# Optimization experiments

Measured on AMD Instinct MI355X. Metric: run time of the kernel, lower is better.

## Reference

```python
import jax, jax.numpy as jnp
import numpy as np

ALPHA = 0.01  # LeakyReLU negative slope
D_OUT = 128   # output_size; a1 is split at this index


def setup_inputs() -> dict:
    key = jax.random.key(0)
    k1, k2, k3, k4 = jax.random.split(key, 4)
    B, N, M, D_IN = 8, 2048, 2048, 256
    input_tensor1 = jax.random.normal(k1, (B, N, D_IN), dtype=jnp.float32)
    input_tensor2 = jax.random.normal(k2, (B, M, D_IN), dtype=jnp.float32)
    attention_mask2 = jnp.zeros((B, 1, M), dtype=jnp.float32)
    # Parameters (xavier-uniform-like scaled normals are fine for a numeric reference)
    W1 = jax.random.normal(k3, (D_IN, D_OUT), dtype=jnp.float32) * (1.414 * np.sqrt(2.0 / (D_IN + D_OUT)))
    a1 = jax.random.normal(k4, (2 * D_OUT, 1), dtype=jnp.float32) * (1.414 * np.sqrt(2.0 / (2 * D_OUT + 1)))
    return {"input_tensor1": input_tensor1, "input_tensor2": input_tensor2,
            "attention_mask2": attention_mask2, "W1": W1, "a1": a1}


def reference(input_tensor1, input_tensor2, attention_mask2, W1, a1):
    # Projections (dropout is identity in eval / p=0)
    Wh1 = jnp.einsum('bnd,de->bne', input_tensor1, W1)  # (B, N, E)
    Wh2 = jnp.einsum('bmd,de->bme', input_tensor2, W1)  # (B, M, E)
    # GAT-style additive score: broadcast outer-sum of two rank-1 projections
    att1 = jnp.einsum('bne,eo->bno', Wh1, a1[:D_OUT, :])   # (B, N, 1)
    att2 = jnp.einsum('bme,eo->bmo', Wh2, a1[D_OUT:, :])   # (B, M, 1)
    e = att1 + jnp.swapaxes(att2, 1, 2)                     # (B, N, M)
    e = jnp.where(e > 0, e, ALPHA * e)                      # LeakyReLU
    scores = e + attention_mask2                            # additive mask
    probs = jax.nn.softmax(scores, axis=-1)                 # (B, N, M)
    context = jnp.einsum('bnm,bme->bne', probs, Wh2)        # (B, N, E)
    return (context, probs)
```

## Files before the change

kernel.cpp:

```cpp
#include <hip/hip_runtime.h>

#define B 8
#define N 2048
#define M 2048
#define DIN 256
#define E 128
#define ALPHA 0.01f

typedef __attribute__((ext_vector_type(8))) short bf16x8;
typedef __attribute__((ext_vector_type(4))) float f32x4;

__device__ inline ushort f2bf(float x) {
  unsigned u = __float_as_uint(x);
  u = (u + 0x7FFFu + ((u >> 16) & 1u)) >> 16;
  return (ushort)u;
}

__global__ __launch_bounds__(256) void prep_v_kernel(
    const float* __restrict__ W1, const float* __restrict__ a1,
    float* __restrict__ v1, float* __restrict__ v2) {
  int k = threadIdx.x;
  float s1 = 0.f, s2 = 0.f;
#pragma unroll 8
  for (int e = 0; e < E; ++e) {
    float w = W1[k * E + e];
    s1 += w * a1[e];
    s2 += w * a1[E + e];
  }
  v1[k] = s1;
  v2[k] = s2;
}

__global__ __launch_bounds__(256) void att_kernel(
    const float* __restrict__ in1, const float* __restrict__ in2,
    const float* __restrict__ v1, const float* __restrict__ v2,
    float* __restrict__ att1, float* __restrict__ att2) {
  int wave = blockIdx.x * 4 + (threadIdx.x >> 6);
  int lane = threadIdx.x & 63;
  const float* src;
  const float* v;
  float* dst;
  int row;
  if (wave < B * N) {
    src = in1; v = v1; dst = att1; row = wave;
  } else {
    src = in2; v = v2; dst = att2; row = wave - B * N;
  }
  float4 x = *(const float4*)(src + (size_t)row * DIN + lane * 4);
  float4 vv = *(const float4*)(v + lane * 4);
  float d = x.x * vv.x + x.y * vv.y + x.z * vv.z + x.w * vv.w;
#pragma unroll
  for (int off = 32; off; off >>= 1) d += __shfl_down(d, off, 64);
  if (lane == 0) dst[row] = d;
}

__global__ __launch_bounds__(256) void wh2_kernel(
    const float* __restrict__ in2, const float* __restrict__ W1,
    ushort* __restrict__ Wb) {
  __shared__ float a[32][DIN];
  int r0 = blockIdx.x * 32;
#pragma unroll
  for (int i = 0; i < 8; ++i) {
    int f = (threadIdx.x + i * 256) * 4;
    int r = f >> 8, k = f & 255;
    *(float4*)&a[r][k] = *(const float4*)(in2 + (size_t)(r0 + r) * DIN + k);
  }
  __syncthreads();
  int c  = (threadIdx.x & 31) * 4;
  int tr = (threadIdx.x >> 5) * 4;
  float acc[4][4] = {};
  for (int k = 0; k < DIN; ++k) {
    float4 b = *(const float4*)(W1 + k * E + c);
#pragma unroll
    for (int r = 0; r < 4; ++r) {
      float av = a[tr + r][k];
      acc[r][0] += av * b.x;
      acc[r][1] += av * b.y;
      acc[r][2] += av * b.z;
      acc[r][3] += av * b.w;
    }
  }
#pragma unroll
  for (int r = 0; r < 4; ++r) {
    int m = r0 + tr + r;
    size_t gbase = (size_t)(m >> 3) * 128 * 8 + (m & 7);
#pragma unroll
    for (int j = 0; j < 4; ++j)
      Wb[gbase + (size_t)(c + j) * 8] = f2bf(acc[r][j]);
  }
}

__global__ __launch_bounds__(256) void softmax_kernel(
    const float* __restrict__ att1, const float* __restrict__ att2,
    const float* __restrict__ mask, float* __restrict__ probs) {
  int row = blockIdx.x;
  int b = row >> 11;
  float a1v = att1[row];
  __shared__ float red[8];
  float s[8];
  float mx = -1e30f;
#pragma unroll
  for (int j = 0; j < 8; ++j) {
    int m = j * 256 + threadIdx.x;
    float t = a1v + att2[b * M + m];
    t = t > 0.f ? t : ALPHA * t;
    t += mask[b * M + m];
    s[j] = t;
    mx = fmaxf(mx, t);
  }
#pragma unroll
  for (int off = 32; off; off >>= 1) mx = fmaxf(mx, __shfl_xor(mx, off, 64));
  int wid = threadIdx.x >> 6;
  if ((threadIdx.x & 63) == 0) red[wid] = mx;
  __syncthreads();
  mx = fmaxf(fmaxf(red[0], red[1]), fmaxf(red[2], red[3]));
  float sum = 0.f;
#pragma unroll
  for (int j = 0; j < 8; ++j) {
    s[j] = __expf(s[j] - mx);
    sum += s[j];
  }
#pragma unroll
  for (int off = 32; off; off >>= 1) sum += __shfl_xor(sum, off, 64);
  if ((threadIdx.x & 63) == 0) red[4 + wid] = sum;
  __syncthreads();
  sum = red[4] + red[5] + red[6] + red[7];
  float inv = 1.f / sum;
#pragma unroll
  for (int j = 0; j < 8; ++j) {
    int m = j * 256 + threadIdx.x;
    probs[(size_t)row * M + m] = s[j] * inv;
  }
}

__global__ __launch_bounds__(256) void context_kernel(
    const float* __restrict__ probs, const ushort* __restrict__ Wb,
    float* __restrict__ ctx) {
  __shared__ short ldsA[32][72];
  __shared__ ushort ldsB[8 * 128 * 8];
  int rt = blockIdx.x & 63;
  int b  = blockIdx.x >> 6;
  int row0 = b * N + rt * 32;
  int t = threadIdx.x;
  int lane = t & 63;
  int w = t >> 6;
  int quad = lane >> 4;
  int l16 = lane & 15;
  int m0w = (w & 1) * 16;
  int n0w = (w >> 1) * 64;
  int ar = t >> 3;
  int ak = (t & 7) * 8;

  f32x4 acc[4] = {};

  for (int k0 = 0; k0 < M; k0 += 64) {
    const float* ap = probs + (size_t)(row0 + ar) * M + k0 + ak;
    float4 p0 = *(const float4*)ap;
    float4 p1 = *(const float4*)(ap + 4);
    bf16x8 av;
    av[0] = (short)f2bf(p0.x); av[1] = (short)f2bf(p0.y);
    av[2] = (short)f2bf(p0.z); av[3] = (short)f2bf(p0.w);
    av[4] = (short)f2bf(p1.x); av[5] = (short)f2bf(p1.y);
    av[6] = (short)f2bf(p1.z); av[7] = (short)f2bf(p1.w);
    *(bf16x8*)&ldsA[ar][ak] = av;
    {
      const char* g =
          (const char*)(Wb + (size_t)(b * 256 + (k0 >> 3)) * 128 * 8);
      char* l = (char*)ldsB;
      int base = w * 4096 + lane * 16;
#pragma unroll
      for (int i = 0; i < 4; ++i) {
        int off = base + i * 1024;
        __builtin_amdgcn_global_load_lds(
            (const __attribute__((address_space(1))) void*)(g + off),
            (__attribute__((address_space(3))) void*)(l + off), 16, 0, 0);
      }
    }
    __syncthreads();
#pragma unroll
    for (int ks = 0; ks < 64; ks += 32) {
      bf16x8 af = *(const bf16x8*)&ldsA[m0w + l16][ks + quad * 8];
      int gl = (ks >> 3) + quad;
#pragma unroll
      for (int cf = 0; cf < 4; ++cf) {
        int n = n0w + cf * 16 + l16;
        bf16x8 bf = *(const bf16x8*)&ldsB[((size_t)gl * 128 + n) * 8];
        acc[cf] =
            __builtin_amdgcn_mfma_f32_16x16x32_bf16(af, bf, acc[cf], 0, 0, 0);
      }
    }
    __syncthreads();
  }
#pragma unroll
  for (int cf = 0; cf < 4; ++cf) {
    int nn = n0w + cf * 16 + l16;
#pragma unroll
    for (int reg = 0; reg < 4; ++reg) {
      int rr = row0 + m0w + quad * 4 + reg;
      ctx[(size_t)rr * E + nn] = acc[cf][reg];
    }
  }
}

extern "C" void kernel_launch(void* const* d_in, const int* in_sizes, int n_in,
                              void* d_out, int out_size, void* d_ws,
                              size_t ws_size, hipStream_t stream) {
  (void)in_sizes; (void)n_in; (void)out_size; (void)ws_size;
  const float* in1  = (const float*)d_in[0];
  const float* in2  = (const float*)d_in[1];
  const float* mask = (const float*)d_in[2];
  const float* W1   = (const float*)d_in[3];
  const float* a1   = (const float*)d_in[4];

  float* ws   = (float*)d_ws;
  float* v1   = ws;
  float* v2   = v1 + DIN;
  float* att1 = v2 + DIN;
  float* att2 = att1 + B * N;
  ushort* Wb  = (ushort*)(att2 + B * M);

  float* ctx   = (float*)d_out;
  float* probs = ctx + (size_t)B * N * E;

  hipLaunchKernelGGL(prep_v_kernel, dim3(1), dim3(256), 0, stream, W1, a1, v1, v2);
  hipLaunchKernelGGL(att_kernel, dim3((B * N + B * M) / 4), dim3(256), 0, stream,
                     in1, in2, v1, v2, att1, att2);
  hipLaunchKernelGGL(wh2_kernel, dim3(B * M / 32), dim3(256), 0, stream,
                     in2, W1, Wb);
  hipLaunchKernelGGL(softmax_kernel, dim3(B * N), dim3(256), 0, stream,
                     att1, att2, mask, probs);
  hipLaunchKernelGGL(context_kernel, dim3(B * N / 32), dim3(256), 0, stream,
                     probs, Wb, ctx);
}
```

Measured before the change: 248.5 us.

## Fuse softmax into context GEMM, recomputing probabilities on the fly

Merges the softmax and context kernels into one kernel. Each block stages the att2 and mask rows in LDS, computes per-row max and sum over 32 rows, then regenerates probabilities inside the MFMA loop. Those values are written to the probs output and converted to bf16 for the A operand, so the full probs matrix is no longer re-read from global memory. In exchange the exp/LeakyReLU work is done three times per element, the LDS footprint grows, and the probs stores come from only half the waves with a strided per-lane pattern.

```diff
diff --git a/kernel.cpp b/kernel.cpp
--- a/kernel.cpp
+++ b/kernel.cpp
@@ -90,79 +90,83 @@
   }
 }
 
-__global__ __launch_bounds__(256) void softmax_kernel(
+__global__ __launch_bounds__(256) void fused_kernel(
     const float* __restrict__ att1, const float* __restrict__ att2,
-    const float* __restrict__ mask, float* __restrict__ probs) {
-  int row = blockIdx.x;
-  int b = row >> 11;
-  float a1v = att1[row];
-  __shared__ float red[8];
-  float s[8];
-  float mx = -1e30f;
-#pragma unroll
-  for (int j = 0; j < 8; ++j) {
-    int m = j * 256 + threadIdx.x;
-    float t = a1v + att2[b * M + m];
-    t = t > 0.f ? t : ALPHA * t;
-    t += mask[b * M + m];
-    s[j] = t;
-    mx = fmaxf(mx, t);
-  }
-#pragma unroll
-  for (int off = 32; off; off >>= 1) mx = fmaxf(mx, __shfl_xor(mx, off, 64));
-  int wid = threadIdx.x >> 6;
-  if ((threadIdx.x & 63) == 0) red[wid] = mx;
-  __syncthreads();
-  mx = fmaxf(fmaxf(red[0], red[1]), fmaxf(red[2], red[3]));
-  float sum = 0.f;
-#pragma unroll
-  for (int j = 0; j < 8; ++j) {
-    s[j] = __expf(s[j] - mx);
-    sum += s[j];
-  }
-#pragma unroll
-  for (int off = 32; off; off >>= 1) sum += __shfl_xor(sum, off, 64);
-  if ((threadIdx.x & 63) == 0) red[4 + wid] = sum;
-  __syncthreads();
-  sum = red[4] + red[5] + red[6] + red[7];
-  float inv = 1.f / sum;
-#pragma unroll
-  for (int j = 0; j < 8; ++j) {
-    int m = j * 256 + threadIdx.x;
-    probs[(size_t)row * M + m] = s[j] * inv;
-  }
-}
-
-__global__ __launch_bounds__(256) void context_kernel(
-    const float* __restrict__ probs, const ushort* __restrict__ Wb,
-    float* __restrict__ ctx) {
-  __shared__ short ldsA[32][72];
+    const float* __restrict__ mask, const ushort* __restrict__ Wb,
+    float* __restrict__ probs, float* __restrict__ ctx) {
+  __shared__ float att2s[M];
+  __shared__ float masks[M];
+  __shared__ float att1s[32];
+  __shared__ float red[32][9];
+  __shared__ float rowmax[32];
+  __shared__ float rowinv[32];
   __shared__ ushort ldsB[8 * 128 * 8];
+
   int rt = blockIdx.x & 63;
   int b  = blockIdx.x >> 6;
   int row0 = b * N + rt * 32;
   int t = threadIdx.x;
+
+#pragma unroll
+  for (int i = 0; i < 2; ++i) {
+    int idx = (t + i * 256) * 4;
+    *(float4*)&att2s[idx] = *(const float4*)(att2 + b * M + idx);
+    *(float4*)&masks[idx] = *(const float4*)(mask + b * M + idx);
+  }
+  if (t < 32) att1s[t] = att1[row0 + t];
+  __syncthreads();
+
+  int r = t >> 3, ch = t & 7;
+  float a1r = att1s[r];
+  float mx = -1e30f;
+  for (int m = ch * 256; m < ch * 256 + 256; ++m) {
+    float s = a1r + att2s[m];
+    s = s > 0.f ? s : ALPHA * s;
+    s += masks[m];
+    mx = fmaxf(mx, s);
+  }
+  red[r][ch] = mx;
+  __syncthreads();
+  if (t < 32) {
+    float m2 = red[t][0];
+#pragma unroll
+    for (int j = 1; j < 8; ++j) m2 = fmaxf(m2, red[t][j]);
+    rowmax[t] = m2;
+  }
+  __syncthreads();
+  float rmax = rowmax[r];
+  float sum = 0.f;
+  for (int m = ch * 256; m < ch * 256 + 256; ++m) {
+    float s = a1r + att2s[m];
+    s = s > 0.f ? s : ALPHA * s;
+    s += masks[m];
+    sum += __expf(s - rmax);
+  }
+  red[r][ch] = sum;
+  __syncthreads();
+  if (t < 32) {
+    float s2 = 0.f;
+#pragma unroll
+    for (int j = 0; j < 8; ++j) s2 += red[t][j];
+    rowinv[t] = 1.f / s2;
+  }
+  __syncthreads();
+
   int lane = t & 63;
   int w = t >> 6;
   int quad = lane >> 4;
   int l16 = lane & 15;
   int m0w = (w & 1) * 16;
   int n0w = (w >> 1) * 64;
-  int ar = t >> 3;
-  int ak = (t & 7) * 8;
+  float a1v  = att1s[m0w + l16];
+  float rmxL = rowmax[m0w + l16];
+  float rinL = rowinv[m0w + l16];
+  bool do_store = (n0w == 0);
+  float* prow = probs + (size_t)(row0 + m0w + l16) * M;
 
   f32x4 acc[4] = {};
 
   for (int k0 = 0; k0 < M; k0 += 64) {
-    const float* ap = probs + (size_t)(row0 + ar) * M + k0 + ak;
-    float4 p0 = *(const float4*)ap;
-    float4 p1 = *(const float4*)(ap + 4);
-    bf16x8 av;
-    av[0] = (short)f2bf(p0.x); av[1] = (short)f2bf(p0.y);
-    av[2] = (short)f2bf(p0.z); av[3] = (short)f2bf(p0.w);
-    av[4] = (short)f2bf(p1.x); av[5] = (short)f2bf(p1.y);
-    av[6] = (short)f2bf(p1.z); av[7] = (short)f2bf(p1.w);
-    *(bf16x8*)&ldsA[ar][ak] = av;
     {
       const char* g =
           (const char*)(Wb + (size_t)(b * 256 + (k0 >> 3)) * 128 * 8);
@@ -179,14 +183,29 @@
     __syncthreads();
 #pragma unroll
     for (int ks = 0; ks < 64; ks += 32) {
-      bf16x8 af = *(const bf16x8*)&ldsA[m0w + l16][ks + quad * 8];
+      int kb = k0 + ks + quad * 8;
+      bf16x8 af;
+      float p[8];
+#pragma unroll
+      for (int j = 0; j < 8; ++j) {
+        float s = a1v + att2s[kb + j];
+        s = s > 0.f ? s : ALPHA * s;
+        s += masks[kb + j];
+        float pe = __expf(s - rmxL) * rinL;
+        p[j] = pe;
+        af[j] = (short)f2bf(pe);
+      }
+      if (do_store) {
+        *(float4*)(prow + kb)     = make_float4(p[0], p[1], p[2], p[3]);
+        *(float4*)(prow + kb + 4) = make_float4(p[4], p[5], p[6], p[7]);
+      }
       int gl = (ks >> 3) + quad;
 #pragma unroll
       for (int cf = 0; cf < 4; ++cf) {
         int n = n0w + cf * 16 + l16;
-        bf16x8 bf = *(const bf16x8*)&ldsB[((size_t)gl * 128 + n) * 8];
+        bf16x8 bfb = *(const bf16x8*)&ldsB[((size_t)gl * 128 + n) * 8];
         acc[cf] =
-            __builtin_amdgcn_mfma_f32_16x16x32_bf16(af, bf, acc[cf], 0, 0, 0);
+            __builtin_amdgcn_mfma_f32_16x16x32_bf16(af, bfb, acc[cf], 0, 0, 0);
       }
     }
     __syncthreads();
@@ -227,8 +246,6 @@
                      in1, in2, v1, v2, att1, att2);
   hipLaunchKernelGGL(wh2_kernel, dim3(B * M / 32), dim3(256), 0, stream,
                      in2, W1, Wb);
-  hipLaunchKernelGGL(softmax_kernel, dim3(B * N), dim3(256), 0, stream,
-                     att1, att2, mask, probs);
-  hipLaunchKernelGGL(context_kernel, dim3(B * N / 32), dim3(256), 0, stream,
-                     probs, Wb, ctx);
-}
+  hipLaunchKernelGGL(fused_kernel, dim3(B * N / 32), dim3(256), 0, stream,
+                     att1, att2, mask, Wb, probs, ctx);
+}
```

Result: slower. 266.7 us (+7.3%).
